# Kernel optimization log

Hardware: AMD Instinct MI355X
Metric: run time of the kernel (lower is better)

The kernel has to match this reference:

```python
import jax, jax.numpy as jnp
import numpy as np

DIM, HEADS, FEAT = 512, 8, 128
HEAD_DIM = DIM // HEADS
B, N = 1, 2048
EPS = 1e-8


def setup_inputs() -> dict:
    key = jax.random.key(0)
    k1, k2, k3, k4 = jax.random.split(key, 4)
    x = jax.random.normal(k1, (B, N, DIM), dtype=jnp.float32)
    proj_matrix = jax.random.normal(k2, (HEADS, HEAD_DIM, FEAT), dtype=jnp.float32) / np.sqrt(HEAD_DIM)
    W_qkv = jax.random.normal(k3, (DIM, 3 * DIM), dtype=jnp.float32) * np.sqrt(2.0 / DIM)
    W_out = jax.random.normal(k4, (DIM, DIM), dtype=jnp.float32) * np.sqrt(2.0 / DIM)
    b_out = jnp.zeros((DIM,), dtype=jnp.float32)
    return {"x": x, "proj_matrix": proj_matrix, "W_qkv": W_qkv, "W_out": W_out, "b_out": b_out}


def _feature_map(t):
    return jax.nn.elu(t) + 1.0


def reference(x, proj_matrix, W_qkv, W_out, b_out):
    b, n, d = x.shape
    h, hd = HEADS, HEAD_DIM
    qkv = x @ W_qkv                      # (b,n,3d)
    q, k, v = jnp.split(qkv, 3, axis=-1)
    # (b,n,d) -> (b,h,n,hd)
    def to_heads(t):
        return t.reshape(b, n, h, hd).transpose(0, 2, 1, 3)
    q, k, v = to_heads(q), to_heads(k), to_heads(v)
    q_proj = _feature_map(jnp.einsum('bhnd,hdf->bhnf', q, proj_matrix))
    k_proj = _feature_map(jnp.einsum('bhnd,hdf->bhnf', k, proj_matrix))
    # causal linear attention via prefix sums (matches torch cumsum branch)
    k_cum = jnp.cumsum(k_proj, axis=2)                                   # (b,h,n,f)
    kv_cum = jnp.cumsum(k_proj[..., None] * v[..., None, :], axis=2)     # (b,h,n,f,hd)
    attn = jnp.einsum('bhnf,bhnfd->bhnd', q_proj, kv_cum)
    denom = jnp.einsum('bhnf,bhnf->bhn', q_proj, k_cum)[..., None]
    attn = attn / (denom + EPS)
    attn = attn.transpose(0, 2, 1, 3).reshape(b, n, d)
    return attn @ W_out + b_out
```

## Files before the change

### kernel.cpp

```cpp
#include <hip/hip_runtime.h>
#include <math.h>

#define NTOK 2048
#define DMODEL 512
#define NH 8
#define HD 64
#define NF 128
#define QKV_LD 1536
#define CHUNK 64
#define NCHUNK 32
#define EPS_C 1e-8f

typedef __bf16 bf16x8 __attribute__((ext_vector_type(8)));
typedef float f32x4 __attribute__((ext_vector_type(4)));

__device__ inline unsigned short f2bf(float f) {
  union { float f; unsigned u; } v; v.f = f;
  unsigned r = v.u + 0x7FFF + ((v.u >> 16) & 1);
  return (unsigned short)(r >> 16);
}


__global__ __launch_bounds__(256) void pack_flat(
    const float* __restrict__ x, const float* __restrict__ W_qkv,
    const float* __restrict__ W_out, const float* __restrict__ proj,
    unsigned short* __restrict__ xpk, unsigned short* __restrict__ wqkvpk,
    unsigned short* __restrict__ woutpk, unsigned short* __restrict__ projpk,
    unsigned short* __restrict__ vT_pk)
{
  const int v = blockIdx.x;
  unsigned short o[8];
  if (v < 512) {
    const int tid = v * 256 + threadIdx.x;
    const int lane = tid & 63, blk = tid >> 6;
    const int bk = blk & 15, bm = blk >> 4;
    const int m = bm * 16 + (lane & 15), k = bk * 32 + (lane >> 4) * 8;
    const float4 v0 = *(const float4*)&x[(size_t)m * 512 + k];
    const float4 v1 = *(const float4*)&x[(size_t)m * 512 + k + 4];
    o[0] = f2bf(v0.x); o[1] = f2bf(v0.y); o[2] = f2bf(v0.z); o[3] = f2bf(v0.w);
    o[4] = f2bf(v1.x); o[5] = f2bf(v1.y); o[6] = f2bf(v1.z); o[7] = f2bf(v1.w);
    *(ushort4*)&xpk[(size_t)tid * 8]     = *(ushort4*)&o[0];
    *(ushort4*)&xpk[(size_t)tid * 8 + 4] = *(ushort4*)&o[4];
  } else if (v < 896) {
    const int tid = (v - 512) * 256 + threadIdx.x;
    const int lane = tid & 63, blk = tid >> 6;
    const int bk = blk & 15, bn = blk >> 4;
    const int n = bn * 16 + (lane & 15), k = bk * 32 + (lane >> 4) * 8;
#pragma unroll
    for (int e = 0; e < 8; ++e) o[e] = f2bf(W_qkv[(size_t)(k + e) * QKV_LD + n]);
    *(ushort4*)&wqkvpk[(size_t)tid * 8]     = *(ushort4*)&o[0];
    *(ushort4*)&wqkvpk[(size_t)tid * 8 + 4] = *(ushort4*)&o[4];
  } else if (v < 1024) {
    const int tid = (v - 896) * 256 + threadIdx.x;
    const int lane = tid & 63, blk = tid >> 6;
    const int bk = blk & 15, bn = blk >> 4;
    const int n = bn * 16 + (lane & 15), k = bk * 32 + (lane >> 4) * 8;
#pragma unroll
    for (int e = 0; e < 8; ++e) o[e] = f2bf(W_out[(size_t)(k + e) * DMODEL + n]);
    *(ushort4*)&woutpk[(size_t)tid * 8]     = *(ushort4*)&o[0];
    *(ushort4*)&woutpk[(size_t)tid * 8 + 4] = *(ushort4*)&o[4];
  } else if (v < 1056) {
    const int tid = (v - 1024) * 256 + threadIdx.x;
    const int lane = tid & 63, blk = (tid >> 6) & 15, h = tid >> 10;
    const int bk = blk & 1, bn = blk >> 1;
    const int n = bn * 16 + (lane & 15), k = bk * 32 + (lane >> 4) * 8;
#pragma unroll
    for (int e = 0; e < 8; ++e) o[e] = f2bf(proj[(size_t)h * HD * NF + (size_t)(k + e) * NF + n]);
    *(ushort4*)&projpk[(size_t)tid * 8]     = *(ushort4*)&o[0];
    *(ushort4*)&projpk[(size_t)tid * 8 + 4] = *(ushort4*)&o[4];
  } else {
    const int tid = (v - 1056) * 256 + threadIdx.x;
    const int hc = tid >> 7, kt = (tid >> 6) & 1, lane = tid & 63;
    const unsigned short val = ((lane & 15) == 0) ? (unsigned short)0x3F80 : (unsigned short)0;
    const size_t u = (size_t)hc * 640 + (4 * 2 + kt) * 64 + lane;
#pragma unroll
    for (int e = 0; e < 8; ++e) o[e] = val;
    *(ushort4*)&vT_pk[u * 8]     = *(ushort4*)&o[0];
    *(ushort4*)&vT_pk[u * 8 + 4] = *(ushort4*)&o[4];
  }
}

__global__ __launch_bounds__(256) void qkv_proj(
    const unsigned short* __restrict__ Apk, const unsigned short* __restrict__ Bpk,
    const unsigned short* __restrict__ projpk,
    unsigned short* __restrict__ q_pk, unsigned short* __restrict__ k_pk,
    unsigned short* __restrict__ kT_pk, unsigned short* __restrict__ vT_pk)
{
  __shared__ unsigned short QK[4096];
  const int lane = threadIdx.x & 63, w = threadIdx.x >> 6;
  const int wr = w >> 1, wc = w & 1;
  const int c = blockIdx.y;
  const int m0 = c * 64 + wr * 32;
  const int n0 = blockIdx.x * 64 + wc * 32;
  const unsigned short* a0 = Apk + ((size_t)(m0 >> 4) * 16 * 64 + lane) * 8;
  const unsigned short* a1 = a0 + (size_t)16 * 512;
  const unsigned short* b0 = Bpk + ((size_t)(n0 >> 4) * 16 * 64 + lane) * 8;
  const unsigned short* b1 = b0 + (size_t)16 * 512;
  f32x4 acc00 = {0.f, 0.f, 0.f, 0.f}, acc01 = acc00, acc10 = acc00, acc11 = acc00;
#pragma unroll 8
  for (int s = 0; s < 16; ++s) {
    const bf16x8 af0 = *(const bf16x8*)(a0 + (size_t)s * 512);
    const bf16x8 af1 = *(const bf16x8*)(a1 + (size_t)s * 512);
    const bf16x8 bv0 = *(const bf16x8*)(b0 + (size_t)s * 512);
    const bf16x8 bv1 = *(const bf16x8*)(b1 + (size_t)s * 512);
    acc00 = __builtin_amdgcn_mfma_f32_16x16x32_bf16(af0, bv0, acc00, 0, 0, 0);
    acc01 = __builtin_amdgcn_mfma_f32_16x16x32_bf16(af0, bv1, acc01, 0, 0, 0);
    acc10 = __builtin_amdgcn_mfma_f32_16x16x32_bf16(af1, bv0, acc10, 0, 0, 0);
    acc11 = __builtin_amdgcn_mfma_f32_16x16x32_bf16(af1, bv1, acc11, 0, 0, 0);
  }
  const int r16 = lane & 15, kg = lane >> 4;
  if (blockIdx.x < 16) {
    const int src = blockIdx.x >> 3, h = blockIdx.x & 7;
#pragma unroll
    for (int mb = 0; mb < 2; ++mb) {
#pragma unroll
      for (int nb = 0; nb < 2; ++nb) {
        const f32x4 a = mb == 0 ? (nb == 0 ? acc00 : acc01) : (nb == 0 ? acc10 : acc11);
        const size_t u = ((size_t)(wr * 2 + mb) * 2 + wc) * 64 +
                         (nb * 2 + (r16 >> 3)) * 16 + kg * 4;
        const int elem = r16 & 7;
#pragma unroll
        for (int r = 0; r < 4; ++r)
          QK[(u + r) * 8 + elem] = f2bf(a[r]);
      }
    }
    __syncthreads();
    const unsigned short* bbase = projpk + (size_t)h * 8192 + (size_t)lane * 8;
    f32x4 p[2][4] = {};
#pragma unroll
    for (int s = 0; s < 2; ++s) {
#pragma unroll
      for (int mb = 0; mb < 2; ++mb) {
        const bf16x8 af = *(const bf16x8*)&QK[((((size_t)(wr * 2 + mb)) * 2 + s) * 64 + lane) * 8];
#pragma unroll
        for (int nb = 0; nb < 4; ++nb) {
          const bf16x8 bv = *(const bf16x8*)(bbase + (size_t)((wc * 4 + nb) * 2 + s) * 512);
          p[mb][nb] = __builtin_amdgcn_mfma_f32_16x16x32_bf16(af, bv, p[mb][nb], 0, 0, 0);
        }
      }
    }
    unsigned short* dst = (src ? k_pk : q_pk) + (size_t)h * 262144;
#pragma unroll
    for (int mb = 0; mb < 2; ++mb) {
#pragma unroll
      for (int nb = 0; nb < 4; ++nb) {
        unsigned short vb[4];
#pragma unroll
        for (int r = 0; r < 4; ++r) {
          const float vv = p[mb][nb][r];
          vb[r] = f2bf(vv > 0.f ? vv + 1.f : expf(vv));
        }
        const size_t base = ((size_t)(c * 4 + wr * 2 + mb) * 4 + wc * 2 + (nb >> 1)) * 64 +
                            ((nb & 1) * 2 + (r16 >> 3)) * 16;
        const int elem = r16 & 7;
#pragma unroll
        for (int r = 0; r < 4; ++r)
          dst[(base + kg * 4 + r) * 8 + elem] = vb[r];
        if (src == 1) {
          const size_t u = (size_t)(h * 32 + c) * 1024 +
              ((size_t)(wc * 4 + nb) * 2 + wr) * 64 + r16 + (mb * 2 + (kg >> 1)) * 16;
          *(ushort4*)&kT_pk[u * 8 + (kg & 1) * 4] = *(ushort4*)&vb[0];
        }
      }
    }
  } else {
    const int h = blockIdx.x - 16;
#pragma unroll
    for (int mb = 0; mb < 2; ++mb) {
#pragma unroll
      for (int nb = 0; nb < 2; ++nb) {
        const f32x4 a = mb == 0 ? (nb == 0 ? acc00 : acc01) : (nb == 0 ? acc10 : acc11);
        const int vc = wc * 32 + nb * 16 + r16;
        const size_t u = (size_t)(h * 32 + c) * 640 +
            ((size_t)(vc >> 4) * 2 + wr) * 64 + (vc & 15) + (mb * 2 + (kg >> 1)) * 16;
        ushort4 rr;
        rr.x = f2bf(a[0]); rr.y = f2bf(a[1]); rr.z = f2bf(a[2]); rr.w = f2bf(a[3]);
        *(ushort4*)&vT_pk[u * 8 + (kg & 1) * 4] = rr;
      }
    }
  }
}

__global__ __launch_bounds__(256) void sums_scan(
    const unsigned short* __restrict__ kT_pk, const unsigned short* __restrict__ vT_pk,
    unsigned short* __restrict__ kvpre_pk)
{
  const int lane = threadIdx.x & 63, w = threadIdx.x >> 6;
  const int vt = blockIdx.x, h = blockIdx.y;
  const int r16 = lane & 15, kg = lane >> 4;
  f32x4 acc[2] = {};
  for (int c = 0; c < NCHUNK; ++c) {
    unsigned short* dst = kvpre_pk + (size_t)(h * 32 + c) * 1280 * 8;
#pragma unroll
    for (int mb = 0; mb < 2; ++mb) {
      unsigned short vb[4];
#pragma unroll
      for (int r = 0; r < 4; ++r) vb[r] = f2bf(acc[mb][r]);
      const size_t u = (size_t)(vt * 4 + w) * 64 + r16 + (mb * 2 + (kg >> 1)) * 16;
      *(ushort4*)&dst[u * 8 + (kg & 1) * 4] = *(ushort4*)&vb[0];
    }
    const unsigned short* kb = kT_pk + (size_t)(h * 32 + c) * 1024 * 8;
    const unsigned short* vb_ = vT_pk + (size_t)(h * 32 + c) * 640 * 8;
#pragma unroll
    for (int s = 0; s < 2; ++s) {
      const bf16x8 bf = *(const bf16x8*)(vb_ + (((size_t)vt * 2 + s) * 64 + lane) * 8);
#pragma unroll
      for (int mb = 0; mb < 2; ++mb) {
        const bf16x8 af = *(const bf16x8*)(kb + ((((size_t)(w * 2 + mb)) * 2 + s) * 64 + lane) * 8);
        acc[mb] = __builtin_amdgcn_mfma_f32_16x16x32_bf16(af, bf, acc[mb], 0, 0, 0);
      }
    }
  }
}

__global__ __launch_bounds__(128) void chunk_attn2(
    const unsigned short* __restrict__ q_pk, const unsigned short* __restrict__ k_pk,
    const unsigned short* __restrict__ kvpre_pk, const unsigned short* __restrict__ vT_pk,
    unsigned short* __restrict__ attn_pk)
{
  __shared__ unsigned short P[2048];
  __shared__ float den[32];
  const int lane = threadIdx.x & 63, wc = threadIdx.x >> 6;
  const int c = blockIdx.x, h = blockIdx.y, rh = blockIdx.z;
  const int r16 = lane & 15, kg = lane >> 4;
  const unsigned short* qb = q_pk + (size_t)h * 262144;
  const unsigned short* kb = k_pk + (size_t)h * 262144;
  bf16x8 qa[2][4];
#pragma unroll
  for (int amb = 0; amb < 2; ++amb)
#pragma unroll
    for (int ks = 0; ks < 4; ++ks)
      qa[amb][ks] = *(const bf16x8*)(qb +
          (((size_t)(c * 4 + rh * 2 + amb) * 4 + ks) * 64 + lane) * 8);
  {
    f32x4 accS[2][2] = {};
#pragma unroll
    for (int ks = 0; ks < 4; ++ks) {
#pragma unroll
      for (int bnb = 0; bnb < 2; ++bnb) {
        const bf16x8 bf = *(const bf16x8*)(kb +
            (((size_t)(c * 4 + wc * 2 + bnb) * 4 + ks) * 64 + lane) * 8);
#pragma unroll
        for (int amb = 0; amb < 2; ++amb)
          accS[amb][bnb] = __builtin_amdgcn_mfma_f32_16x16x32_bf16(qa[amb][ks], bf, accS[amb][bnb], 0, 0, 0);
      }
    }
#pragma unroll
    for (int amb = 0; amb < 2; ++amb)
#pragma unroll
      for (int bnb = 0; bnb < 2; ++bnb) {
        const int ck = wc * 32 + bnb * 16 + r16;
        const size_t u = ((size_t)amb * 2 + wc) * 64 + (bnb * 2 + (r16 >> 3)) * 16;
        const int elem = r16 & 7;
#pragma unroll
        for (int r = 0; r < 4; ++r) {
          const int rq = rh * 32 + amb * 16 + kg * 4 + r;
          P[(u + kg * 4 + r) * 8 + elem] = (ck <= rq) ? f2bf(accS[amb][bnb][r]) : (unsigned short)0;
        }
      }
  }
  __syncthreads();
  const int nnt = wc ? 2 : 3;
  const int ntb = wc ? 3 : 0;
  const unsigned short* kvp = kvpre_pk + (size_t)(h * 32 + c) * 1280 * 8;
  const unsigned short* vtb = vT_pk + (size_t)(h * 32 + c) * 640 * 8;
  f32x4 acc[2][3] = {};
#pragma unroll
  for (int ks = 0; ks < 4; ++ks) {
    bf16x8 bfr[3];
    for (int jj = 0; jj < 3; ++jj)
      if (jj < nnt)
        bfr[jj] = *(const bf16x8*)(kvp + (((size_t)(ntb + jj) * 4 + ks) * 64 + lane) * 8);
#pragma unroll
    for (int amb = 0; amb < 2; ++amb)
      for (int jj = 0; jj < 3; ++jj)
        if (jj < nnt)
          acc[amb][jj] = __builtin_amdgcn_mfma_f32_16x16x32_bf16(qa[amb][ks], bfr[jj], acc[amb][jj], 0, 0, 0);
  }
#pragma unroll
  for (int ks = 0; ks < 2; ++ks) {
    bf16x8 bfr[3];
    for (int jj = 0; jj < 3; ++jj)
      if (jj < nnt)
        bfr[jj] = *(const bf16x8*)(vtb + (((size_t)(ntb + jj) * 2 + ks) * 64 + lane) * 8);
#pragma unroll
    for (int amb = 0; amb < 2; ++amb) {
      const bf16x8 pf = *(const bf16x8*)&P[(((size_t)amb * 2 + ks) * 64 + lane) * 8];
      for (int jj = 0; jj < 3; ++jj)
        if (jj < nnt)
          acc[amb][jj] = __builtin_amdgcn_mfma_f32_16x16x32_bf16(pf, bfr[jj], acc[amb][jj], 0, 0, 0);
    }
  }
  if (wc == 1 && r16 == 0) {
#pragma unroll
    for (int amb = 0; amb < 2; ++amb)
#pragma unroll
      for (int r = 0; r < 4; ++r)
        den[amb * 16 + kg * 4 + r] = acc[amb][1][r] + EPS_C;
  }
  __syncthreads();
#pragma unroll
  for (int amb = 0; amb < 2; ++amb) {
    for (int jj = 0; jj < 3; ++jj) {
      const int nt = ntb + jj;
      if (nt >= 4 || jj >= nnt) continue;
      const int acol = h * 64 + nt * 16 + r16;
      const size_t base = ((size_t)(c * 4 + rh * 2 + amb) * 16 + (acol >> 5)) * 64 +
                          ((nt * 2 + (r16 >> 3)) & 3) * 16;
      const int elem = acol & 7;
#pragma unroll
      for (int r = 0; r < 4; ++r) {
        const float dinv = 1.0f / den[amb * 16 + kg * 4 + r];
        attn_pk[(base + kg * 4 + r) * 8 + elem] = f2bf(acc[amb][jj][r] * dinv);
      }
    }
  }
}

__global__ __launch_bounds__(256) void gemm_out(
    const unsigned short* __restrict__ Apk, const unsigned short* __restrict__ Bpk,
    const float* __restrict__ bias, float* __restrict__ Cf, int K, int ldc)
{
  const int lane = threadIdx.x & 63, w = threadIdx.x >> 6;
  const int wr = w >> 1, wc = w & 1;
  const int m0 = blockIdx.y * 64 + wr * 32;
  const int n0 = blockIdx.x * 64 + wc * 32;
  const int ks = K >> 5;
  const unsigned short* a0 = Apk + ((size_t)(m0 >> 4) * ks * 64 + lane) * 8;
  const unsigned short* a1 = a0 + (size_t)ks * 512;
  const unsigned short* b0 = Bpk + ((size_t)(n0 >> 4) * ks * 64 + lane) * 8;
  const unsigned short* b1 = b0 + (size_t)ks * 512;
  f32x4 acc00 = {0.f, 0.f, 0.f, 0.f}, acc01 = acc00, acc10 = acc00, acc11 = acc00;
#pragma unroll 8
  for (int s = 0; s < ks; ++s) {
    const bf16x8 af0 = *(const bf16x8*)(a0 + (size_t)s * 512);
    const bf16x8 af1 = *(const bf16x8*)(a1 + (size_t)s * 512);
    const bf16x8 bv0 = *(const bf16x8*)(b0 + (size_t)s * 512);
    const bf16x8 bv1 = *(const bf16x8*)(b1 + (size_t)s * 512);
    acc00 = __builtin_amdgcn_mfma_f32_16x16x32_bf16(af0, bv0, acc00, 0, 0, 0);
    acc01 = __builtin_amdgcn_mfma_f32_16x16x32_bf16(af0, bv1, acc01, 0, 0, 0);
    acc10 = __builtin_amdgcn_mfma_f32_16x16x32_bf16(af1, bv0, acc10, 0, 0, 0);
    acc11 = __builtin_amdgcn_mfma_f32_16x16x32_bf16(af1, bv1, acc11, 0, 0, 0);
  }
  const int r16 = lane & 15, kg = lane >> 4;
#pragma unroll
  for (int mb = 0; mb < 2; ++mb) {
#pragma unroll
    for (int nb = 0; nb < 2; ++nb) {
      const f32x4 a = mb == 0 ? (nb == 0 ? acc00 : acc01) : (nb == 0 ? acc10 : acc11);
      const int col = n0 + nb * 16 + r16;
      const float bv = bias[col];
#pragma unroll
      for (int r = 0; r < 4; ++r)
        Cf[(size_t)(m0 + mb * 16 + kg * 4 + r) * ldc + col] = a[r] + bv;
    }
  }
}

extern "C" void kernel_launch(void* const* d_in, const int* in_sizes, int n_in,
                              void* d_out, int out_size, void* d_ws, size_t ws_size,
                              hipStream_t stream) {
  const float* x     = (const float*)d_in[0];
  const float* proj  = (const float*)d_in[1];
  const float* W_qkv = (const float*)d_in[2];
  const float* W_out = (const float*)d_in[3];
  const float* b_out = (const float*)d_in[4];
  float* out = (float*)d_out;

  unsigned short* xpk      = (unsigned short*)d_ws;
  unsigned short* wqkvpk   = xpk + 1048576;
  unsigned short* woutpk   = wqkvpk + 786432;
  unsigned short* projpk   = woutpk + 262144;
  unsigned short* q_pk     = projpk + 65536;
  unsigned short* k_pk     = q_pk + 2097152;
  unsigned short* kT_pk    = k_pk + 2097152;
  unsigned short* vT_pk    = kT_pk + 2097152;
  unsigned short* kvpre_pk = vT_pk + 1310720;
  unsigned short* attn_pk  = kvpre_pk + 2621440;

  pack_flat<<<dim3(1184), 256, 0, stream>>>(x, W_qkv, W_out, proj,
                                            xpk, wqkvpk, woutpk, projpk, vT_pk);
  qkv_proj<<<dim3(QKV_LD / 64, NTOK / 64), 256, 0, stream>>>(
      xpk, wqkvpk, projpk, q_pk, k_pk, kT_pk, vT_pk);
  sums_scan<<<dim3(5, NH), 256, 0, stream>>>(kT_pk, vT_pk, kvpre_pk);
  chunk_attn2<<<dim3(NCHUNK, NH, 2), 128, 0, stream>>>(
      q_pk, k_pk, kvpre_pk, vT_pk, attn_pk);
  gemm_out<<<dim3(DMODEL / 64, NTOK / 64), 256, 0, stream>>>(
      attn_pk, woutpk, b_out, out, DMODEL, DMODEL);
}
```

Before: 53.19 us.

## Fuse prefix KV scan into chunk attention by recomputing prefix sums per block

Removes the separate sums_scan kernel and the kvpre workspace. Each attention block now recomputes its prefix K^T V (plus the ones column used for the denominator) by looping over all earlier chunks, keeps the result in shared memory, and handles both row halves in one 256-thread block. The ones-column init of vT moves from pack_flat into qkv_proj. This drops one launch and the serial scan kernel that ran on only 40 blocks, at the cost of redundant prefix work that is quadratic in the chunk count and uneven load across blocks.

```diff
diff --git a/kernel.cpp b/kernel.cpp
--- a/kernel.cpp
+++ b/kernel.cpp
@@ -25,8 +25,7 @@
     const float* __restrict__ x, const float* __restrict__ W_qkv,
     const float* __restrict__ W_out, const float* __restrict__ proj,
     unsigned short* __restrict__ xpk, unsigned short* __restrict__ wqkvpk,
-    unsigned short* __restrict__ woutpk, unsigned short* __restrict__ projpk,
-    unsigned short* __restrict__ vT_pk)
+    unsigned short* __restrict__ woutpk, unsigned short* __restrict__ projpk)
 {
   const int v = blockIdx.x;
   unsigned short o[8];
@@ -59,7 +58,7 @@
     for (int e = 0; e < 8; ++e) o[e] = f2bf(W_out[(size_t)(k + e) * DMODEL + n]);
     *(ushort4*)&woutpk[(size_t)tid * 8]     = *(ushort4*)&o[0];
     *(ushort4*)&woutpk[(size_t)tid * 8 + 4] = *(ushort4*)&o[4];
-  } else if (v < 1056) {
+  } else {
     const int tid = (v - 1024) * 256 + threadIdx.x;
     const int lane = tid & 63, blk = (tid >> 6) & 15, h = tid >> 10;
     const int bk = blk & 1, bn = blk >> 1;
@@ -68,15 +67,6 @@
     for (int e = 0; e < 8; ++e) o[e] = f2bf(proj[(size_t)h * HD * NF + (size_t)(k + e) * NF + n]);
     *(ushort4*)&projpk[(size_t)tid * 8]     = *(ushort4*)&o[0];
     *(ushort4*)&projpk[(size_t)tid * 8 + 4] = *(ushort4*)&o[4];
-  } else {
-    const int tid = (v - 1056) * 256 + threadIdx.x;
-    const int hc = tid >> 7, kt = (tid >> 6) & 1, lane = tid & 63;
-    const unsigned short val = ((lane & 15) == 0) ? (unsigned short)0x3F80 : (unsigned short)0;
-    const size_t u = (size_t)hc * 640 + (4 * 2 + kt) * 64 + lane;
-#pragma unroll
-    for (int e = 0; e < 8; ++e) o[e] = val;
-    *(ushort4*)&vT_pk[u * 8]     = *(ushort4*)&o[0];
-    *(ushort4*)&vT_pk[u * 8 + 4] = *(ushort4*)&o[4];
   }
 }
 
@@ -178,51 +168,62 @@
         *(ushort4*)&vT_pk[u * 8 + (kg & 1) * 4] = rr;
       }
     }
-  }
-}
-
-__global__ __launch_bounds__(256) void sums_scan(
+    if (threadIdx.x < 128) {
+      const int kt = threadIdx.x >> 6, ln = threadIdx.x & 63;
+      const unsigned short val = ((ln & 15) == 0) ? (unsigned short)0x3F80 : (unsigned short)0;
+      unsigned short o8[8];
+#pragma unroll
+      for (int e = 0; e < 8; ++e) o8[e] = val;
+      const size_t u = (size_t)(h * 32 + c) * 640 + (8 + kt) * 64 + ln;
+      *(ushort4*)&vT_pk[u * 8]     = *(ushort4*)&o8[0];
+      *(ushort4*)&vT_pk[u * 8 + 4] = *(ushort4*)&o8[4];
+    }
+  }
+}
+
+__global__ __launch_bounds__(256) void attn_fused(
+    const unsigned short* __restrict__ q_pk, const unsigned short* __restrict__ k_pk,
     const unsigned short* __restrict__ kT_pk, const unsigned short* __restrict__ vT_pk,
-    unsigned short* __restrict__ kvpre_pk)
-{
-  const int lane = threadIdx.x & 63, w = threadIdx.x >> 6;
-  const int vt = blockIdx.x, h = blockIdx.y;
-  const int r16 = lane & 15, kg = lane >> 4;
-  f32x4 acc[2] = {};
-  for (int c = 0; c < NCHUNK; ++c) {
-    unsigned short* dst = kvpre_pk + (size_t)(h * 32 + c) * 1280 * 8;
-#pragma unroll
-    for (int mb = 0; mb < 2; ++mb) {
-      unsigned short vb[4];
-#pragma unroll
-      for (int r = 0; r < 4; ++r) vb[r] = f2bf(acc[mb][r]);
-      const size_t u = (size_t)(vt * 4 + w) * 64 + r16 + (mb * 2 + (kg >> 1)) * 16;
-      *(ushort4*)&dst[u * 8 + (kg & 1) * 4] = *(ushort4*)&vb[0];
-    }
-    const unsigned short* kb = kT_pk + (size_t)(h * 32 + c) * 1024 * 8;
-    const unsigned short* vb_ = vT_pk + (size_t)(h * 32 + c) * 640 * 8;
-#pragma unroll
-    for (int s = 0; s < 2; ++s) {
-      const bf16x8 bf = *(const bf16x8*)(vb_ + (((size_t)vt * 2 + s) * 64 + lane) * 8);
-#pragma unroll
-      for (int mb = 0; mb < 2; ++mb) {
-        const bf16x8 af = *(const bf16x8*)(kb + ((((size_t)(w * 2 + mb)) * 2 + s) * 64 + lane) * 8);
-        acc[mb] = __builtin_amdgcn_mfma_f32_16x16x32_bf16(af, bf, acc[mb], 0, 0, 0);
-      }
-    }
-  }
-}
-
-__global__ __launch_bounds__(128) void chunk_attn2(
-    const unsigned short* __restrict__ q_pk, const unsigned short* __restrict__ k_pk,
-    const unsigned short* __restrict__ kvpre_pk, const unsigned short* __restrict__ vT_pk,
     unsigned short* __restrict__ attn_pk)
 {
-  __shared__ unsigned short P[2048];
-  __shared__ float den[32];
-  const int lane = threadIdx.x & 63, wc = threadIdx.x >> 6;
-  const int c = blockIdx.x, h = blockIdx.y, rh = blockIdx.z;
+  __shared__ unsigned short KV[10240];
+  __shared__ unsigned short P[4096];
+  __shared__ float den[64];
+  const int lane = threadIdx.x & 63, w = threadIdx.x >> 6;
+  const int wr = w >> 1, wc = w & 1;
+  const int c = blockIdx.x, h = blockIdx.y;
   const int r16 = lane & 15, kg = lane >> 4;
+
+  f32x4 acc2[2][5] = {};
+  for (int cc = 0; cc < c; ++cc) {
+    const unsigned short* kb_ = kT_pk + (size_t)(h * 32 + cc) * 1024 * 8;
+    const unsigned short* vb_ = vT_pk + (size_t)(h * 32 + cc) * 640 * 8;
+#pragma unroll
+    for (int s = 0; s < 2; ++s) {
+      bf16x8 bfr[5];
+#pragma unroll
+      for (int nt = 0; nt < 5; ++nt)
+        bfr[nt] = *(const bf16x8*)(vb_ + (((size_t)nt * 2 + s) * 64 + lane) * 8);
+#pragma unroll
+      for (int mb = 0; mb < 2; ++mb) {
+        const bf16x8 af = *(const bf16x8*)(kb_ + ((((size_t)(w * 2 + mb)) * 2 + s) * 64 + lane) * 8);
+#pragma unroll
+        for (int nt = 0; nt < 5; ++nt)
+          acc2[mb][nt] = __builtin_amdgcn_mfma_f32_16x16x32_bf16(af, bfr[nt], acc2[mb][nt], 0, 0, 0);
+      }
+    }
+  }
+#pragma unroll
+  for (int mb = 0; mb < 2; ++mb)
+#pragma unroll
+    for (int nt = 0; nt < 5; ++nt) {
+      unsigned short vb4[4];
+#pragma unroll
+      for (int r = 0; r < 4; ++r) vb4[r] = f2bf(acc2[mb][nt][r]);
+      const size_t u = (size_t)(nt * 4 + w) * 64 + r16 + (mb * 2 + (kg >> 1)) * 16;
+      *(ushort4*)&KV[u * 8 + (kg & 1) * 4] = *(ushort4*)&vb4[0];
+    }
+
   const unsigned short* qb = q_pk + (size_t)h * 262144;
   const unsigned short* kb = k_pk + (size_t)h * 262144;
   bf16x8 qa[2][4];
@@ -231,7 +232,7 @@
 #pragma unroll
     for (int ks = 0; ks < 4; ++ks)
       qa[amb][ks] = *(const bf16x8*)(qb +
-          (((size_t)(c * 4 + rh * 2 + amb) * 4 + ks) * 64 + lane) * 8);
+          (((size_t)(c * 4 + wr * 2 + amb) * 4 + ks) * 64 + lane) * 8);
   {
     f32x4 accS[2][2] = {};
 #pragma unroll
@@ -250,11 +251,11 @@
 #pragma unroll
       for (int bnb = 0; bnb < 2; ++bnb) {
         const int ck = wc * 32 + bnb * 16 + r16;
-        const size_t u = ((size_t)amb * 2 + wc) * 64 + (bnb * 2 + (r16 >> 3)) * 16;
+        const size_t u = ((size_t)(wr * 2 + amb) * 2 + wc) * 64 + (bnb * 2 + (r16 >> 3)) * 16;
         const int elem = r16 & 7;
 #pragma unroll
         for (int r = 0; r < 4; ++r) {
-          const int rq = rh * 32 + amb * 16 + kg * 4 + r;
+          const int rq = wr * 32 + amb * 16 + kg * 4 + r;
           P[(u + kg * 4 + r) * 8 + elem] = (ck <= rq) ? f2bf(accS[amb][bnb][r]) : (unsigned short)0;
         }
       }
@@ -262,7 +263,6 @@
   __syncthreads();
   const int nnt = wc ? 2 : 3;
   const int ntb = wc ? 3 : 0;
-  const unsigned short* kvp = kvpre_pk + (size_t)(h * 32 + c) * 1280 * 8;
   const unsigned short* vtb = vT_pk + (size_t)(h * 32 + c) * 640 * 8;
   f32x4 acc[2][3] = {};
 #pragma unroll
@@ -270,7 +270,7 @@
     bf16x8 bfr[3];
     for (int jj = 0; jj < 3; ++jj)
       if (jj < nnt)
-        bfr[jj] = *(const bf16x8*)(kvp + (((size_t)(ntb + jj) * 4 + ks) * 64 + lane) * 8);
+        bfr[jj] = *(const bf16x8*)&KV[(((size_t)(ntb + jj) * 4 + ks) * 64 + lane) * 8];
 #pragma unroll
     for (int amb = 0; amb < 2; ++amb)
       for (int jj = 0; jj < 3; ++jj)
@@ -285,7 +285,7 @@
         bfr[jj] = *(const bf16x8*)(vtb + (((size_t)(ntb + jj) * 2 + ks) * 64 + lane) * 8);
 #pragma unroll
     for (int amb = 0; amb < 2; ++amb) {
-      const bf16x8 pf = *(const bf16x8*)&P[(((size_t)amb * 2 + ks) * 64 + lane) * 8];
+      const bf16x8 pf = *(const bf16x8*)&P[((((size_t)(wr * 2 + amb)) * 2 + ks) * 64 + lane) * 8];
       for (int jj = 0; jj < 3; ++jj)
         if (jj < nnt)
           acc[amb][jj] = __builtin_amdgcn_mfma_f32_16x16x32_bf16(pf, bfr[jj], acc[amb][jj], 0, 0, 0);
@@ -296,7 +296,7 @@
     for (int amb = 0; amb < 2; ++amb)
 #pragma unroll
       for (int r = 0; r < 4; ++r)
-        den[amb * 16 + kg * 4 + r] = acc[amb][1][r] + EPS_C;
+        den[wr * 32 + amb * 16 + kg * 4 + r] = acc[amb][1][r] + EPS_C;
   }
   __syncthreads();
 #pragma unroll
@@ -305,12 +305,12 @@
       const int nt = ntb + jj;
       if (nt >= 4 || jj >= nnt) continue;
       const int acol = h * 64 + nt * 16 + r16;
-      const size_t base = ((size_t)(c * 4 + rh * 2 + amb) * 16 + (acol >> 5)) * 64 +
+      const size_t base = ((size_t)(c * 4 + wr * 2 + amb) * 16 + (acol >> 5)) * 64 +
                           ((nt * 2 + (r16 >> 3)) & 3) * 16;
       const int elem = acol & 7;
 #pragma unroll
       for (int r = 0; r < 4; ++r) {
-        const float dinv = 1.0f / den[amb * 16 + kg * 4 + r];
+        const float dinv = 1.0f / den[wr * 32 + amb * 16 + kg * 4 + r];
         attn_pk[(base + kg * 4 + r) * 8 + elem] = f2bf(acc[amb][jj][r] * dinv);
       }
     }
@@ -375,16 +375,14 @@
   unsigned short* k_pk     = q_pk + 2097152;
   unsigned short* kT_pk    = k_pk + 2097152;
   unsigned short* vT_pk    = kT_pk + 2097152;
-  unsigned short* kvpre_pk = vT_pk + 1310720;
-  unsigned short* attn_pk  = kvpre_pk + 2621440;
-
-  pack_flat<<<dim3(1184), 256, 0, stream>>>(x, W_qkv, W_out, proj,
-                                            xpk, wqkvpk, woutpk, projpk, vT_pk);
+  unsigned short* attn_pk  = vT_pk + 1310720;
+
+  pack_flat<<<dim3(1056), 256, 0, stream>>>(x, W_qkv, W_out, proj,
+                                            xpk, wqkvpk, woutpk, projpk);
   qkv_proj<<<dim3(QKV_LD / 64, NTOK / 64), 256, 0, stream>>>(
       xpk, wqkvpk, projpk, q_pk, k_pk, kT_pk, vT_pk);
-  sums_scan<<<dim3(5, NH), 256, 0, stream>>>(kT_pk, vT_pk, kvpre_pk);
-  chunk_attn2<<<dim3(NCHUNK, NH, 2), 128, 0, stream>>>(
-      q_pk, k_pk, kvpre_pk, vT_pk, attn_pk);
+  attn_fused<<<dim3(NCHUNK, NH), 256, 0, stream>>>(
+      q_pk, k_pk, kT_pk, vT_pk, attn_pk);
   gemm_out<<<dim3(DMODEL / 64, NTOK / 64), 256, 0, stream>>>(
       attn_pk, woutpk, b_out, out, DMODEL, DMODEL);
 }
```

Result: slower. 78.19 us (+47.0%).
